# Kernel optimization log

Measured on AMD Instinct MI355X. Metric: run time of the kernel, lower is better.

The kernel has to match this reference:

```python
import jax, jax.numpy as jnp
import numpy as np

B, N_NODE, N_TOK = 8, 512, 8
N_PATHS, PATH_LEN = 256, 64
VOCAB, H = 50000, 256


def gru_dir(x, w_ih, w_hh, b_ih, b_hh):
    # x: [batch, T, H_in] -> [batch, T, H]; PyTorch GRU gate math
    xw = jnp.einsum('bti,gi->btg', x, w_ih) + b_ih  # precompute input-side gates
    h0 = jnp.zeros((x.shape[0], w_hh.shape[1]), x.dtype)
    def step(h, xt):
        gh = h @ w_hh.T + b_hh
        xr, xz, xn = jnp.split(xt, 3, -1)
        hr, hz, hn = jnp.split(gh, 3, -1)
        r = jax.nn.sigmoid(xr + hr)
        z = jax.nn.sigmoid(xz + hz)
        n = jnp.tanh(xn + r * hn)
        h_new = (1.0 - z) * n + z * h
        return h_new, h_new
    _, ys = jax.lax.scan(step, h0, jnp.swapaxes(xw, 0, 1))
    return jnp.swapaxes(ys, 0, 1)


def gru_bidir(x, wf_ih, wf_hh, bf_ih, bf_hh, wb_ih, wb_hh, bb_ih, bb_hh):
    f = gru_dir(x, wf_ih, wf_hh, bf_ih, bf_hh)
    b = jnp.flip(gru_dir(jnp.flip(x, 1), wb_ih, wb_hh, bb_ih, bb_hh), 1)
    return jnp.concatenate([f, b], -1)


def setup_inputs():
    key = jax.random.key(0)
    ks = jax.random.split(key, 18)
    g = lambda k, s: jax.random.normal(k, s, jnp.float32) * 0.06
    return {
        'nodes': jax.random.randint(ks[0], (B, N_NODE, N_TOK), 0, VOCAB),
        'paths': jax.random.randint(ks[1], (B, N_PATHS, PATH_LEN), 0, N_NODE + 1),
        'emb': g(ks[2], (VOCAB, H)),
        'wf_ih': g(ks[3], (3 * H, H)), 'wf_hh': g(ks[4], (3 * H, H)),
        'bf_ih': g(ks[5], (3 * H,)), 'bf_hh': g(ks[6], (3 * H,)),
        'wb_ih': g(ks[7], (3 * H, H)), 'wb_hh': g(ks[8], (3 * H, H)),
        'bb_ih': g(ks[9], (3 * H,)), 'bb_hh': g(ks[10], (3 * H,)),
        'w_transit': g(ks[11], (2 * H, H)), 'b_transit': g(ks[12], (2 * H,)),
        'w_rank': g(ks[13], (2 * H, 2 * H + 1)), 'b_rank': g(ks[14], (2 * H,)),
        'w_h': g(ks[15], (H, 2 * H)), 'b_h': g(ks[16], (H,)),
    }


def reference(nodes, paths, emb, wf_ih, wf_hh, bf_ih, bf_hh, wb_ih, wb_hh, bb_ih, bb_hh, w_transit, b_transit, w_rank, b_rank, w_h, b_h):
    gru = (wf_ih, wf_hh, bf_ih, bf_hh, wb_ih, wb_hh, bb_ih, bb_hh)
    x = jnp.max(emb[nodes], axis=2)                 # [B, N_NODE, H] token max-pool
    base_v = gru_bidir(x, *gru)                     # [B, N_NODE, 2H]
    x_pad = jnp.concatenate([x, jnp.zeros((B, 1, H), x.dtype)], axis=1)
    gathered = jax.vmap(lambda xp, p: xp[p])(x_pad, paths)        # [B, P, L, H]
    nx = gru_bidir(gathered.reshape(B * N_PATHS, PATH_LEN, H), *gru)
    nx = nx.reshape(B, N_PATHS, PATH_LEN, 2 * H)
    # extra rank feature: 1/(path_index+1), broadcast over path positions
    rank = (1.0 / (jnp.arange(N_PATHS, dtype=x.dtype) + 1.0))[None, :, None, None]
    rank = jnp.broadcast_to(rank, (B, N_PATHS, PATH_LEN, 1))
    nx = jnp.concatenate([nx, rank], -1) @ w_rank.T + b_rank      # rank_proj
    p_flat = paths.reshape(B, -1)
    v_flat = nx.reshape(B, N_PATHS * PATH_LEN, 2 * H)
    def pool(pf, vf, xb):
        # scatter-max per node id; id N_NODE is the padding row and is dropped
        vmax = jnp.full((N_NODE + 1, 2 * H), -jnp.inf, vf.dtype).at[pf].max(vf)
        has = jnp.zeros((N_NODE + 1,), bool).at[pf].set(True)
        fallback = xb @ w_transit.T + b_transit
        return jnp.where(has[:N_NODE, None], vmax[:N_NODE], fallback)
    v = jax.vmap(pool)(p_flat, v_flat, x)           # [B, N_NODE, 2H]
    all_v = base_v + v
    last_state = jnp.max(all_v, axis=1) @ w_h.T + b_h             # h_proj branch (GRU -> not tuple)
    return all_v, last_state
```

## Files before the change

kernel.cpp:

```cpp
#include <hip/hip_runtime.h>


#define HH 256
#define NNODE 512
#define PLEN 64

typedef __attribute__((ext_vector_type(8))) short short8;
typedef __attribute__((ext_vector_type(4))) float f32x4;
typedef unsigned short ushort_t;
typedef __attribute__((address_space(1))) const void* gas_t;
typedef __attribute__((address_space(3))) void* las_t;

__device__ __forceinline__ f32x4 mfma16(short8 a, short8 b, f32x4 c) {
    return __builtin_amdgcn_mfma_f32_16x16x32_bf16(a, b, c, 0, 0, 0);
}
__device__ __forceinline__ ushort_t f2bf(float f) {
    unsigned u = __float_as_uint(f);
    u += 0x7fffu + ((u >> 16) & 1u);
    return (ushort_t)(u >> 16);
}
__device__ __forceinline__ float bf2f(ushort_t s) {
    return __uint_as_float(((unsigned)s) << 16);
}
__device__ __forceinline__ float sigm(float x) {
    return __builtin_amdgcn_rcpf(1.f + __expf(-x));
}
__device__ __forceinline__ float tanh_(float x) {
    return 1.f - 2.f * __builtin_amdgcn_rcpf(__expf(2.f * x) + 1.f);
}
__device__ __forceinline__ unsigned fkey(float f) {
    unsigned u = __float_as_uint(f);
    return (u & 0x80000000u) ? ~u : (u | 0x80000000u);
}
__device__ __forceinline__ float fdec(unsigned k) {
    unsigned u = (k & 0x80000000u) ? (k ^ 0x80000000u) : ~k;
    return __uint_as_float(u);
}

__device__ __forceinline__ int xw3_remap(int c) {
    const int dir = c >= 768;
    const int cd = c - dir * 768;
    const int g = cd >> 8, cc = cd & 255;
    const int w2 = cc >> 5, within = cc & 31;
    return dir * 768 + w2 * 96 + (within >> 1) * 6 + g * 2 + (within & 1);
}

__global__ void k_embed(const int* __restrict__ nodes, const float* __restrict__ emb,
                        float* __restrict__ x, ushort_t* __restrict__ xbf)
{
    const int bn = blockIdx.x, h = threadIdx.x;
    const int* nd = nodes + bn * 8;
    float m = -3.4e38f;
#pragma unroll
    for (int k = 0; k < 8; ++k)
        m = fmaxf(m, emb[(size_t)nd[k] * HH + h]);
    x[(size_t)bn * HH + h] = m;
    xbf[(size_t)bn * HH + h] = f2bf(m);
}

__global__ void k_pack(const float* __restrict__ wf_ih, const float* __restrict__ wf_hh,
                       const float* __restrict__ bf_ih, const float* __restrict__ bf_hh,
                       const float* __restrict__ wb_ih, const float* __restrict__ wb_hh,
                       const float* __restrict__ bb_ih, const float* __restrict__ bb_hh,
                       const float* __restrict__ w_rank,
                       ushort_t* __restrict__ whhp, ushort_t* __restrict__ wih_bt,
                       ushort_t* __restrict__ wr_bt, float* __restrict__ rank_l,
                       float* __restrict__ bias2, ushort_t* __restrict__ xw3)
{
    int i = blockIdx.x * 256 + threadIdx.x;
    if (i < 393216) {
        const int e = i & 7, l = (i >> 3) & 63;
        int c = i >> 9;
        const int n = c & 1; c >>= 1;
        const int g = c % 3; c /= 3;
        const int kt = c & 7; c >>= 3;
        const int w2 = c & 7;
        const int dir = c >> 3;
        const float* whh = dir ? wb_hh : wf_hh;
        whhp[i] = f2bf(whh[(g * 256 + w2 * 32 + 2 * (l & 15) + n) * 256 +
                           kt * 32 + (l >> 4) * 8 + e]);
        return;
    }
    i -= 393216;
    if (i < 393216) {
        const int n = i >> 8, k = i & 255;
        const float* wih = (n < 768) ? wf_ih : wb_ih;
        wih_bt[i] = f2bf(wih[(n % 768) * 256 + k]);
        return;
    }
    i -= 393216;
    if (i < 262144) { wr_bt[i] = f2bf(w_rank[(i >> 9) * 513 + (i & 511)]); return; }
    i -= 262144;
    if (i < 512) { rank_l[i] = w_rank[i * 513 + 512]; return; }
    i -= 512;
    if (i < 1536) {
        const int c = i;
        const int dir = c >= 768;
        const int cd = c - dir * 768;
        const int g = cd >> 8;
        const float bi = dir ? bb_ih[cd] : bf_ih[cd];
        const float bh = (g < 2) ? (dir ? bb_hh[cd] : bf_hh[cd]) : 0.f;
        bias2[c] = bi + bh;
        xw3[(size_t)4096 * 1536 + xw3_remap(c)] = f2bf(bi + bh);
    }
}

template<int KD>
__device__ __forceinline__ void gemm_loop(const ushort_t* __restrict__ A,
                                          const ushort_t* __restrict__ Bt,
                                          ushort_t* al, ushort_t* bl,
                                          int bm, int bn, f32x4 acc[4][4])
{
    const int tid = threadIdx.x, w = tid >> 6, l = tid & 63;
    const int lm = l & 15, lh = l >> 4;
    const int wm = w >> 1, wn = w & 1;
    const int lr = l >> 3, lc = (l & 7) * 8;
    for (int k0 = 0; k0 < KD; k0 += 64) {
#pragma unroll
        for (int i = 0; i < 4; ++i) {
            const int c = w * 4 + i;
            const ushort_t* ga = A + (size_t)(bm + c * 8 + lr) * KD + k0 + lc;
            const ushort_t* gb = Bt + (size_t)(bn + c * 8 + lr) * KD + k0 + lc;
            __builtin_amdgcn_global_load_lds((gas_t)ga, (las_t)(al + c * 512), 16, 0, 0);
            __builtin_amdgcn_global_load_lds((gas_t)gb, (las_t)(bl + c * 512), 16, 0, 0);
        }
        __syncthreads();
#pragma unroll
        for (int kt = 0; kt < 2; ++kt) {
            short8 af[4], bfr[4];
            const int ko = kt * 32 + lh * 8;
#pragma unroll
            for (int m = 0; m < 4; ++m)
                af[m] = *(const short8*)(al + (wm * 64 + m * 16 + lm) * 64 + ko);
#pragma unroll
            for (int n = 0; n < 4; ++n)
                bfr[n] = *(const short8*)(bl + (wn * 64 + n * 16 + lm) * 64 + ko);
#pragma unroll
            for (int m = 0; m < 4; ++m)
#pragma unroll
                for (int n = 0; n < 4; ++n)
                    acc[m][n] = mfma16(af[m], bfr[n], acc[m][n]);
        }
        __syncthreads();
    }
}

__global__ void __launch_bounds__(256, 2)
k_gemm_xw(const ushort_t* __restrict__ xbf, const ushort_t* __restrict__ wih_bt,
          const float* __restrict__ bias2, ushort_t* __restrict__ xw3)
{
    __shared__ __align__(16) ushort_t al[128 * 64], bl[128 * 64];
    f32x4 acc[4][4] = {};
    const int bm = blockIdx.y * 128, bn = blockIdx.x * 128;
    gemm_loop<256>(xbf, wih_bt, al, bl, bm, bn, acc);
    const int tid = threadIdx.x, w = tid >> 6, l = tid & 63;
    const int lm = l & 15, lh = l >> 4, wm = w >> 1, wn = w & 1;
#pragma unroll
    for (int m = 0; m < 4; ++m)
#pragma unroll
        for (int rr = 0; rr < 4; ++rr) {
            const int row = bm + wm * 64 + m * 16 + lh * 4 + rr;
#pragma unroll
            for (int n = 0; n < 4; ++n) {
                const int col = bn + wn * 64 + n * 16 + lm;
                xw3[(size_t)row * 1536 + xw3_remap(col)] = f2bf(acc[m][n][rr] + bias2[col]);
            }
        }
}

template<bool IS_BASE>
__device__ __forceinline__ void scan_run(int dir, int sg, int tid,
    const ushort_t* __restrict__ xw3, const ushort_t* __restrict__ whhp,
    const float* __restrict__ bhh, ushort_t (*hl)[4096], const int* idr,
    ushort_t* __restrict__ nx, float* __restrict__ base_v)
{
    const int w = tid >> 6, l = tid & 63;
    const int lm = l & 15, lh = l >> 4;
    const int nsteps = IS_BASE ? NNODE : PLEN;

    short8 Bf[8][3][2];
    {
        const ushort_t* wp = whhp + (size_t)(dir * 8 + w) * 24576 + l * 8;
#pragma unroll
        for (int kt = 0; kt < 8; ++kt)
#pragma unroll
            for (int g = 0; g < 3; ++g)
#pragma unroll
                for (int n = 0; n < 2; ++n) {
                    short8 v = *(const short8*)(wp + (kt * 6 + g * 2 + n) * 512);
                    asm volatile("" : "+a"(v));
                    Bf[kt][g][n] = v;
                }
    }
    const float bn0 = bhh[512 + w * 32 + lm * 2];
    const float bn1 = bhh[512 + w * 32 + lm * 2 + 1];

    __syncthreads();
    for (int i = tid; i < 4096; i += 512) hl[0][i] = 0;
    __syncthreads();

    int cur = 0;
    for (int step = 0; step < nsteps; ++step) {
        const int t = dir ? (nsteps - 1 - step) : step;
        uint3 gv[4];
#pragma unroll
        for (int ri = 0; ri < 4; ++ri) {
            const int sq = lh * 4 + ri;
            const int row = IS_BASE ? ((sq < 8) ? ((sq << 9) + t) : 4096)
                                    : idr[(sq << 6) + t];
            gv[ri] = *(const uint3*)((const char*)xw3 +
                (size_t)row * 3072 + dir * 1536 + w * 192 + lm * 12);
        }
        f32x4 acc[3][2] = {};
        const char* hb = (const char*)hl[cur];
#pragma unroll
        for (int kt = 0; kt < 8; ++kt) {
            const short8 a = *(const short8*)(hb + lm * 512 +
                ((kt * 64 + lh * 16) ^ ((lm & 7) << 4)));
#pragma unroll
            for (int g = 0; g < 3; ++g)
#pragma unroll
                for (int n = 0; n < 2; ++n)
                    acc[g][n] = mfma16(a, Bf[kt][g][n], acc[g][n]);
        }
        ushort_t* hn_ = hl[cur ^ 1];
#pragma unroll
        for (int ri = 0; ri < 4; ++ri) {
            const int sq = lh * 4 + ri;
            const unsigned hv = *(const unsigned*)(hb + sq * 512 +
                ((w * 64 + lm * 4) ^ ((sq & 7) << 4)));
            unsigned hpack = 0;
            float hs0 = 0.f, hs1 = 0.f;
#pragma unroll
            for (int n = 0; n < 2; ++n) {
                const float xr = bf2f((ushort_t)(n ? (gv[ri].x >> 16) : (gv[ri].x & 0xffffu)));
                const float xz = bf2f((ushort_t)(n ? (gv[ri].y >> 16) : (gv[ri].y & 0xffffu)));
                const float xn = bf2f((ushort_t)(n ? (gv[ri].z >> 16) : (gv[ri].z & 0xffffu)));
                const float hov = bf2f((ushort_t)(n ? (hv >> 16) : (hv & 0xffffu)));
                const float rr = sigm(acc[0][n][ri] + xr);
                const float zz = sigm(acc[1][n][ri] + xz);
                const float nn = tanh_(xn + rr * (acc[2][n][ri] + (n ? bn1 : bn0)));
                const float h = (1.f - zz) * nn + zz * hov;
                if (n) hs1 = h; else hs0 = h;
                hpack |= ((unsigned)f2bf(h)) << (n * 16);
            }
            *(unsigned*)((char*)hn_ + sq * 512 + ((w * 64 + lm * 4) ^ ((sq & 7) << 4))) = hpack;
            if (IS_BASE) {
                if (sq < 8)
                    *(float2*)(base_v + ((size_t)(sq * NNODE + t)) * 512 +
                               dir * 256 + w * 32 + lm * 2) = make_float2(hs0, hs1);
            } else {
                *(unsigned*)((char*)nx + (((size_t)((sg * 16 + sq) * PLEN + t)) * 512 +
                    dir * 256 + w * 32 + lm * 2) * 2) = hpack;
            }
        }
        __syncthreads();
        cur ^= 1;
    }
}

__global__ void __launch_bounds__(512)
__attribute__((amdgpu_waves_per_eu(2, 2)))
k_scan(const int* __restrict__ paths, const ushort_t* __restrict__ xw3,
       const ushort_t* __restrict__ whhp,
       const float* __restrict__ bf_hh, const float* __restrict__ bb_hh,
       const ushort_t* __restrict__ wr_bt, const float* __restrict__ b_rank,
       const float* __restrict__ rank_l,
       ushort_t* __restrict__ nx, float* __restrict__ base_v,
       unsigned* __restrict__ keys)
{
    __shared__ __align__(16) ushort_t hl[2][4096];
    __shared__ __align__(16) ushort_t al[8192], bl[8192];
    __shared__ int idr[1024];
    const int tid = threadIdx.x;
    const int w = tid >> 6, l = tid & 63;
    const int lm = l & 15, lh = l >> 4;

    if (blockIdx.x < 2) {
        scan_run<true>((int)blockIdx.x, 0, tid, xw3, whhp,
                       blockIdx.x ? bb_hh : bf_hh, hl, nullptr, nx, base_v);
        return;
    }
    const int sg = (int)blockIdx.x - 2;
    for (int i = tid; i < 1024; i += 512) {
        const int s = sg * 16 + (i >> 6), t = i & 63;
        const int id = paths[(s << 6) + t];
        idr[i] = (id < NNODE) ? (((s >> 8) << 9) + id) : 4096;
    }
    scan_run<false>(0, sg, tid, xw3, whhp, bf_hh, hl, idr, nx, base_v);
    scan_run<false>(1, sg, tid, xw3, whhp, bb_hh, hl, idr, nx, base_v);

    __threadfence_block();
    __syncthreads();
    const int wm = w >> 2, wn = w & 3;
#pragma unroll 1
    for (int job = 0; job < 32; ++job) {
        const int mt = job >> 2, ntile = job & 3;
        const size_t ar0 = (size_t)sg * 1024 + mt * 128;
        const int n0 = ntile * 128;
        f32x4 racc[4][2] = {};
        for (int k0 = 0; k0 < 512; k0 += 64) {
#pragma unroll
            for (int i = 0; i < 2; ++i) {
                const int c = w * 128 + i * 64 + l;
                const int row = c >> 3, j = c & 7;
                const int jp = j ^ (row & 7);
                __builtin_amdgcn_global_load_lds(
                    (gas_t)(nx + (ar0 + row) * 512 + k0 + jp * 8),
                    (las_t)(al + c * 8), 16, 0, 0);
                __builtin_amdgcn_global_load_lds(
                    (gas_t)(wr_bt + (size_t)(n0 + row) * 512 + k0 + jp * 8),
                    (las_t)(bl + c * 8), 16, 0, 0);
            }
            __syncthreads();
#pragma unroll
            for (int kt = 0; kt < 2; ++kt) {
                short8 av[4], bv[2];
#pragma unroll
                for (int m = 0; m < 4; ++m) {
                    const int r = wm * 64 + m * 16 + lm;
                    av[m] = *(const short8*)((const char*)al + r * 128 +
                            ((kt * 64 + lh * 16) ^ ((r & 7) << 4)));
                }
#pragma unroll
                for (int n = 0; n < 2; ++n) {
                    const int r = wn * 32 + n * 16 + lm;
                    bv[n] = *(const short8*)((const char*)bl + r * 128 +
                            ((kt * 64 + lh * 16) ^ ((r & 7) << 4)));
                }
#pragma unroll
                for (int m = 0; m < 4; ++m)
#pragma unroll
                    for (int n = 0; n < 2; ++n)
                        racc[m][n] = mfma16(av[m], bv[n], racc[m][n]);
            }
            __syncthreads();
        }
#pragma unroll
        for (int m = 0; m < 4; ++m)
#pragma unroll
            for (int rr = 0; rr < 4; ++rr) {
                const size_t grow = ar0 + wm * 64 + m * 16 + lh * 4 + rr;
                const int id = paths[grow];
                const float rv = __builtin_amdgcn_rcpf((float)(((grow >> 6) & 255) + 1));
                unsigned* kp = keys + (((grow >> 14) * 513 + id) << 9);
#pragma unroll
                for (int n = 0; n < 2; ++n) {
                    const int col = n0 + wn * 32 + n * 16 + lm;
                    const float v = racc[m][n][rr] + b_rank[col] + rank_l[col] * rv;
                    if (id < NNODE) {
                        const unsigned key = fkey(v);
                        if (key > kp[col]) atomicMax(kp + col, key);
                    }
                }
            }
    }
}

__global__ void k_merge(const unsigned* __restrict__ keys, const float* __restrict__ base_v,
                        const float* __restrict__ x, const float* __restrict__ w_transit,
                        const float* __restrict__ b_transit, float* __restrict__ out0)
{
    const int blk = blockIdx.x;
    const int b = blk >> 9, n = blk & 511;
    const int tid = threadIdx.x;
#pragma unroll
    for (int h = 0; h < 2; ++h) {
        const int o = tid + h * 256;
        const unsigned k = keys[((size_t)(b * 513 + n)) * 512 + o];
        float v;
        if (k) {
            v = fdec(k);
        } else {
            float a = b_transit[o];
            const float* wt = w_transit + o * HH;
            const float* xr = x + ((size_t)(b * NNODE + n)) * HH;
            for (int i = 0; i < HH; ++i) a += xr[i] * wt[i];
            v = a;
        }
        const size_t oi = ((size_t)(b * NNODE + n)) * 512 + o;
        out0[oi] = base_v[oi] + v;
    }
}

__global__ void k_last(const float* __restrict__ out0, const float* __restrict__ w_h,
                       const float* __restrict__ b_h, float* __restrict__ out1)
{
    __shared__ float m[512];
    const int b = blockIdx.x, tid = threadIdx.x;
#pragma unroll
    for (int h = 0; h < 2; ++h) {
        const int o = tid + h * 256;
        float mm = -3.4e38f;
        for (int n = 0; n < NNODE; ++n)
            mm = fmaxf(mm, out0[((size_t)(b * NNODE + n)) * 512 + o]);
        m[o] = mm;
    }
    __syncthreads();
    float a = b_h[tid];
    const float* wr = w_h + tid * 512;
    for (int j = 0; j < 512; ++j) a += m[j] * wr[j];
    out1[b * HH + tid] = a;
}

extern "C" void kernel_launch(void* const* d_in, const int* in_sizes, int n_in,
                              void* d_out, int out_size, void* d_ws, size_t ws_size,
                              hipStream_t stream)
{
    (void)in_sizes; (void)n_in; (void)out_size; (void)ws_size;
    const int* nodes = (const int*)d_in[0];
    const int* paths = (const int*)d_in[1];
    const float* emb = (const float*)d_in[2];
    const float* wf_ih = (const float*)d_in[3];
    const float* wf_hh = (const float*)d_in[4];
    const float* bf_ih = (const float*)d_in[5];
    const float* bf_hh = (const float*)d_in[6];
    const float* wb_ih = (const float*)d_in[7];
    const float* wb_hh = (const float*)d_in[8];
    const float* bb_ih = (const float*)d_in[9];
    const float* bb_hh = (const float*)d_in[10];
    const float* w_transit = (const float*)d_in[11];
    const float* b_transit = (const float*)d_in[12];
    const float* w_rank = (const float*)d_in[13];
    const float* b_rank = (const float*)d_in[14];
    const float* w_h = (const float*)d_in[15];
    const float* b_h = (const float*)d_in[16];

    char* ws = (char*)d_ws;
    float* x = (float*)(ws);
    ushort_t* xbf = (ushort_t*)(ws + 4194304);
    ushort_t* xw3 = (ushort_t*)(ws + 6291456);
    ushort_t* whhp = (ushort_t*)(ws + 18877440);
    ushort_t* wih_bt = (ushort_t*)(ws + 19663872);
    ushort_t* wr_bt = (ushort_t*)(ws + 20450304);
    float* rank_l = (float*)(ws + 20974592);
    float* bias2 = (float*)(ws + 20976640);
    unsigned* keys = (unsigned*)(ws + 20982784);
    float* base_v = (float*)(ws + 29387776);
    ushort_t* nx = (ushort_t*)(ws + 37776384);

    float* out0 = (float*)d_out;
    float* out1 = out0 + 2097152;

    hipMemsetAsync(keys, 0, 8404992, stream);
    k_embed<<<4096, 256, 0, stream>>>(nodes, emb, x, xbf);
    k_pack<<<4104, 256, 0, stream>>>(wf_ih, wf_hh, bf_ih, bf_hh, wb_ih, wb_hh,
                                     bb_ih, bb_hh, w_rank,
                                     whhp, wih_bt, wr_bt, rank_l, bias2, xw3);
    k_gemm_xw<<<dim3(12, 32), 256, 0, stream>>>(xbf, wih_bt, bias2, xw3);
    k_scan<<<130, 512, 0, stream>>>(paths, xw3, whhp, bf_hh, bb_hh, wr_bt,
                                    b_rank, rank_l, nx, base_v, keys);
    k_merge<<<4096, 256, 0, stream>>>(keys, base_v, x, w_transit, b_transit, out0);
    k_last<<<8, 256, 0, stream>>>(out0, w_h, b_h, out1);
}
```

Before: 2.011 ms.

## Split recurrent GRU weights across VGPRs, LDS, and streamed global loads

The scan kernel previously kept all 48 W_hh MFMA fragments per wave pinned in AGPRs and forced two waves per EU. Now 12 fragments stay in VGPRs, 16 are staged once into a 128KB LDS buffer via global_load_lds, and the remaining 20 are re-read from global/L2 each timestep, with the weight pack reordered to match. The waves_per_eu attribute is dropped and the LDS buffer is reused for the rank-projection tiles. This lowers register pressure but adds LDS reads and per-step global loads on the serial recurrence critical path.

Result: faster. 1.887 ms (-6.2%).

```diff
diff --git a/kernel.cpp b/kernel.cpp
--- a/kernel.cpp
+++ b/kernel.cpp
@@ -70,12 +70,17 @@
     int i = blockIdx.x * 256 + threadIdx.x;
     if (i < 393216) {
         const int e = i & 7, l = (i >> 3) & 63;
-        int c = i >> 9;
-        const int n = c & 1; c >>= 1;
-        const int g = c % 3; c /= 3;
-        const int kt = c & 7; c >>= 3;
-        const int w2 = c & 7;
-        const int dir = c >> 3;
+        const int c = i >> 9;
+        const int q = c % 48;
+        const int w2 = (c / 48) & 7;
+        const int dir = c / 384;
+        int kt, g;
+        if (q < 12)      { kt = q / 6;            g = (q % 6) >> 1; }
+        else if (q < 24) { kt = 2 + (q - 12) / 6; g = ((q - 12) % 6) >> 1; }
+        else if (q < 28) { kt = 4;                g = (q - 24) >> 1; }
+        else if (q < 30) { kt = 4;                g = 2; }
+        else             { kt = 5 + (q - 30) / 6; g = ((q - 30) % 6) >> 1; }
+        const int n = q & 1;
         const float* whh = dir ? wb_hh : wf_hh;
         whhp[i] = f2bf(whh[(g * 256 + w2 * 32 + 2 * (l & 15) + n) * 256 +
                            kt * 32 + (l >> 4) * 8 + e]);
@@ -171,27 +176,27 @@
 template<bool IS_BASE>
 __device__ __forceinline__ void scan_run(int dir, int sg, int tid,
     const ushort_t* __restrict__ xw3, const ushort_t* __restrict__ whhp,
-    const float* __restrict__ bhh, ushort_t (*hl)[4096], const int* idr,
+    const float* __restrict__ bhh, ushort_t* __restrict__ wl,
+    ushort_t (*hl)[4096], const int* idr,
     ushort_t* __restrict__ nx, float* __restrict__ base_v)
 {
     const int w = tid >> 6, l = tid & 63;
     const int lm = l & 15, lh = l >> 4;
     const int nsteps = IS_BASE ? NNODE : PLEN;
-
-    short8 Bf[8][3][2];
-    {
-        const ushort_t* wp = whhp + (size_t)(dir * 8 + w) * 24576 + l * 8;
-#pragma unroll
-        for (int kt = 0; kt < 8; ++kt)
-#pragma unroll
-            for (int g = 0; g < 3; ++g)
-#pragma unroll
-                for (int n = 0; n < 2; ++n) {
-                    short8 v = *(const short8*)(wp + (kt * 6 + g * 2 + n) * 512);
-                    asm volatile("" : "+a"(v));
-                    Bf[kt][g][n] = v;
-                }
-    }
+    const ushort_t* wp = whhp + ((size_t)(dir * 8 + w) * 48) * 512 + l * 8;
+
+    short8 Breg[12];
+#pragma unroll
+    for (int q = 0; q < 12; ++q) {
+        short8 v = *(const short8*)(wp + q * 512);
+        asm volatile("" : "+v"(v));
+        Breg[q] = v;
+    }
+#pragma unroll
+    for (int q = 12; q < 28; ++q)
+        __builtin_amdgcn_global_load_lds((gas_t)(wp + q * 512),
+            (las_t)(wl + ((q - 12) * 8 + w) * 512), 16, 0, 0);
+
     const float bn0 = bhh[512 + w * 32 + lm * 2];
     const float bn1 = bhh[512 + w * 32 + lm * 2 + 1];
 
@@ -211,18 +216,55 @@
             gv[ri] = *(const uint3*)((const char*)xw3 +
                 (size_t)row * 3072 + dir * 1536 + w * 192 + lm * 12);
         }
+        short8 st[8];
+#pragma unroll
+        for (int j = 0; j < 8; ++j) st[j] = *(const short8*)(wp + (28 + j) * 512);
+
         f32x4 acc[3][2] = {};
         const char* hb = (const char*)hl[cur];
-#pragma unroll
-        for (int kt = 0; kt < 8; ++kt) {
-            const short8 a = *(const short8*)(hb + lm * 512 +
-                ((kt * 64 + lh * 16) ^ ((lm & 7) << 4)));
-#pragma unroll
-            for (int g = 0; g < 3; ++g)
-#pragma unroll
-                for (int n = 0; n < 2; ++n)
-                    acc[g][n] = mfma16(a, Bf[kt][g][n], acc[g][n]);
-        }
+        short8 af;
+#pragma unroll
+        for (int kt = 0; kt < 2; ++kt) {
+            af = *(const short8*)(hb + lm * 512 + ((kt * 64 + lh * 16) ^ ((lm & 7) << 4)));
+#pragma unroll
+            for (int j = 0; j < 6; ++j)
+                acc[j >> 1][j & 1] = mfma16(af, Breg[kt * 6 + j], acc[j >> 1][j & 1]);
+        }
+#pragma unroll
+        for (int kt = 2; kt < 4; ++kt) {
+            af = *(const short8*)(hb + lm * 512 + ((kt * 64 + lh * 16) ^ ((lm & 7) << 4)));
+            const int fb = (kt - 2) * 6;
+#pragma unroll
+            for (int j = 0; j < 6; ++j) {
+                const short8 b = *(const short8*)(wl + ((fb + j) * 8 + w) * 512 + l * 8);
+                acc[j >> 1][j & 1] = mfma16(af, b, acc[j >> 1][j & 1]);
+            }
+        }
+        af = *(const short8*)(hb + lm * 512 + ((4 * 64 + lh * 16) ^ ((lm & 7) << 4)));
+#pragma unroll
+        for (int j = 0; j < 4; ++j) {
+            const short8 b = *(const short8*)(wl + ((12 + j) * 8 + w) * 512 + l * 8);
+            acc[j >> 1][j & 1] = mfma16(af, b, acc[j >> 1][j & 1]);
+        }
+        acc[2][0] = mfma16(af, st[0], acc[2][0]);
+        acc[2][1] = mfma16(af, st[1], acc[2][1]);
+        af = *(const short8*)(hb + lm * 512 + ((5 * 64 + lh * 16) ^ ((lm & 7) << 4)));
+#pragma unroll
+        for (int j = 0; j < 6; ++j)
+            acc[j >> 1][j & 1] = mfma16(af, st[2 + j], acc[j >> 1][j & 1]);
+#pragma unroll
+        for (int j = 0; j < 6; ++j) st[2 + j] = *(const short8*)(wp + (36 + j) * 512);
+        af = *(const short8*)(hb + lm * 512 + ((6 * 64 + lh * 16) ^ ((lm & 7) << 4)));
+#pragma unroll
+        for (int j = 0; j < 6; ++j)
+            acc[j >> 1][j & 1] = mfma16(af, st[2 + j], acc[j >> 1][j & 1]);
+#pragma unroll
+        for (int j = 0; j < 6; ++j) st[2 + j] = *(const short8*)(wp + (42 + j) * 512);
+        af = *(const short8*)(hb + lm * 512 + ((7 * 64 + lh * 16) ^ ((lm & 7) << 4)));
+#pragma unroll
+        for (int j = 0; j < 6; ++j)
+            acc[j >> 1][j & 1] = mfma16(af, st[2 + j], acc[j >> 1][j & 1]);
+
         ushort_t* hn_ = hl[cur ^ 1];
 #pragma unroll
         for (int ri = 0; ri < 4; ++ri) {
@@ -260,7 +302,6 @@
 }
 
 __global__ void __launch_bounds__(512)
-__attribute__((amdgpu_waves_per_eu(2, 2)))
 k_scan(const int* __restrict__ paths, const ushort_t* __restrict__ xw3,
        const ushort_t* __restrict__ whhp,
        const float* __restrict__ bf_hh, const float* __restrict__ bb_hh,
@@ -269,8 +310,8 @@
        ushort_t* __restrict__ nx, float* __restrict__ base_v,
        unsigned* __restrict__ keys)
 {
+    __shared__ __align__(16) ushort_t wl[65536];
     __shared__ __align__(16) ushort_t hl[2][4096];
-    __shared__ __align__(16) ushort_t al[8192], bl[8192];
     __shared__ int idr[1024];
     const int tid = threadIdx.x;
     const int w = tid >> 6, l = tid & 63;
@@ -278,7 +319,7 @@
 
     if (blockIdx.x < 2) {
         scan_run<true>((int)blockIdx.x, 0, tid, xw3, whhp,
-                       blockIdx.x ? bb_hh : bf_hh, hl, nullptr, nx, base_v);
+                       blockIdx.x ? bb_hh : bf_hh, wl, hl, nullptr, nx, base_v);
         return;
     }
     const int sg = (int)blockIdx.x - 2;
@@ -287,11 +328,13 @@
         const int id = paths[(s << 6) + t];
         idr[i] = (id < NNODE) ? (((s >> 8) << 9) + id) : 4096;
     }
-    scan_run<false>(0, sg, tid, xw3, whhp, bf_hh, hl, idr, nx, base_v);
-    scan_run<false>(1, sg, tid, xw3, whhp, bb_hh, hl, idr, nx, base_v);
+    scan_run<false>(0, sg, tid, xw3, whhp, bf_hh, wl, hl, idr, nx, base_v);
+    scan_run<false>(1, sg, tid, xw3, whhp, bb_hh, wl, hl, idr, nx, base_v);
 
     __threadfence_block();
     __syncthreads();
+    ushort_t* al = wl;
+    ushort_t* bl = wl + 8192;
     const int wm = w >> 2, wn = w & 3;
 #pragma unroll 1
     for (int job = 0; job < 32; ++job) {
```
